# Optimization experiments

Hardware: AMD Instinct MI355X
Metric: run time of the kernel (lower is better)

## Reference

```python
import jax, jax.numpy as jnp
import numpy as np

B, T, F, H, O = 16384, 128, 9, 128, 12


def setup_inputs() -> dict:
    key = jax.random.key(0)
    ks = jax.random.split(key, 14)
    s = 1.0 / np.sqrt(H)
    u = lambda k, shp: jax.random.uniform(k, shp, jnp.float32, -s, s)
    return {
        "x": jax.random.normal(ks[0], (B, T, F), jnp.float32),
        "W_in": u(ks[1], (H, F)), "b_in": u(ks[2], (H,)),
        "Wih0": u(ks[3], (4 * H, H)), "Whh0": u(ks[4], (4 * H, H)),
        "bih0": u(ks[5], (4 * H,)), "bhh0": u(ks[6], (4 * H,)),
        "Wih1": u(ks[7], (4 * H, H)), "Whh1": u(ks[8], (4 * H, H)),
        "bih1": u(ks[9], (4 * H,)), "bhh1": u(ks[10], (4 * H,)),
        "W_out": u(ks[11], (O, H)), "b_out": u(ks[12], (O,)),
    }


def _cell(h, c, xp, Wih, Whh, bih, bhh):
    # PyTorch LSTM gate order: i, f, g, o
    g = xp @ Wih.T + bih + h @ Whh.T + bhh  # [B, 4H]
    i, f, gg, o = jnp.split(g, 4, axis=-1)
    c = jax.nn.sigmoid(f) * c + jax.nn.sigmoid(i) * jnp.tanh(gg)
    h = jax.nn.sigmoid(o) * jnp.tanh(c)
    return h, c


def reference(x, W_in, b_in, Wih0, Whh0, bih0, bhh0, Wih1, Whh1, bih1, bhh1, W_out, b_out):
    # input projection, all timesteps at once: [B, T, H] -> scan over time
    xp = jnp.einsum('btf,hf->tbh', x, W_in) + b_in
    b = x.shape[0]
    zeros = jnp.zeros((b, H), x.dtype)
    carry0 = (zeros, zeros, zeros, zeros)  # h0, c0, h1, c1

    def step(carry, xt):
        h0, c0, h1, c1 = carry
        h0, c0 = _cell(h0, c0, xt, Wih0, Whh0, bih0, bhh0)
        h1, c1 = _cell(h1, c1, h0, Wih1, Whh1, bih1, bhh1)
        return (h0, c0, h1, c1), None

    (h0, c0, h1, c1), _ = jax.lax.scan(step, carry0, xp)
    # torch forward returns only the LAST step's output: out(h1) with softmax over dim=1
    return jax.nn.softmax(h1 @ W_out.T + b_out, axis=1)
```

## Files before the change

kernel.cpp:

```cpp
#include <hip/hip_runtime.h>
#include <stdint.h>
#include <stddef.h>

#define T_STEPS 128
#define F_IN 9
#define HID 128
#define OUT_N 12
#define XROW (T_STEPS * F_IN)

typedef __attribute__((ext_vector_type(8))) short bf16x8;
typedef __attribute__((ext_vector_type(4))) float f32x4;

#define MFMA16(a, b, c) __builtin_amdgcn_mfma_f32_16x16x32_bf16((a), (b), (c), 0, 0, 0)

__device__ __forceinline__ short f2bf(float f) {
  union { float f; uint32_t u; } v; v.f = f;
  return (short)((v.u + 0x7fffu + ((v.u >> 16) & 1u)) >> 16);
}
__device__ __forceinline__ float frcp(float x) { return __builtin_amdgcn_rcpf(x); }
__device__ __forceinline__ float sigm(float x) {
  return frcp(1.0f + __builtin_amdgcn_exp2f(-1.4426950408889634f * x));
}
__device__ __forceinline__ float tanh_f(float x) {
  return 1.0f - 2.0f * frcp(1.0f + __builtin_amdgcn_exp2f(2.8853900817779268f * x));
}

__global__ void prep_w0x(const float* __restrict__ W_in, const float* __restrict__ b_in,
                         const float* __restrict__ Wih0, const float* __restrict__ bih0,
                         const float* __restrict__ bhh0, const float* __restrict__ bih1,
                         const float* __restrict__ bhh1,
                         short* __restrict__ w0xf, float* __restrict__ b0x, float* __restrict__ b1) {
  int tid = threadIdx.x;
  int nt = tid >> 4, hl = tid & 15;
  int w = nt >> 2, g = nt & 3;
  int n = g * 128 + w * 16 + hl;
  float wacc[F_IN];
#pragma unroll
  for (int f = 0; f < F_IN; ++f) wacc[f] = 0.f;
  float bacc = 0.f;
  for (int h = 0; h < HID; ++h) {
    float wv = Wih0[n * HID + h];
    bacc += wv * b_in[h];
#pragma unroll
    for (int f = 0; f < F_IN; ++f) wacc[f] += wv * W_in[h * F_IN + f];
  }
  b0x[n] = bacc + bih0[n] + bhh0[n];
  b1[n] = bih1[n] + bhh1[n];
#pragma unroll
  for (int k = 0; k < 32; ++k) {
    int quad = k >> 3, j = k & 7;
    w0xf[((w * 4 + g) * 64 + quad * 16 + hl) * 8 + j] = (k < F_IN) ? f2bf(wacc[k]) : (short)0;
  }
}

__global__ void prep_wrec(const float* __restrict__ Whh0, const float* __restrict__ Wih1,
                          const float* __restrict__ Whh1,
                          short* __restrict__ whh0f, short* __restrict__ w1f) {
  int gt = blockIdx.x * blockDim.x + threadIdx.x;
  if (gt < 2048) {
    int kt = gt >> 9, rr = gt & 511;
    int nt = rr >> 4, hl = rr & 15;
    int w = nt >> 2, g = nt & 3;
    int n = g * 128 + w * 16 + hl;
#pragma unroll
    for (int k = 0; k < 32; ++k) {
      int quad = k >> 3, j = k & 7;
      whh0f[((w * 16 + kt * 4 + g) * 64 + quad * 16 + hl) * 8 + j] =
          f2bf(Whh0[n * HID + kt * 32 + k]);
    }
  } else {
    int g2 = gt - 2048;
    int kt = g2 >> 9, rr = g2 & 511;
    int nt = rr >> 4, hl = rr & 15;
    int w = nt >> 2, g = nt & 3;
    int n = g * 128 + w * 16 + hl;
#pragma unroll
    for (int k = 0; k < 32; ++k) {
      int quad = k >> 3, j = k & 7;
      int kg = kt * 32 + k;
      float v = (kg < HID) ? Wih1[n * HID + kg] : Whh1[n * HID + kg - HID];
      w1f[((w * 32 + kt * 4 + g) * 64 + quad * 16 + hl) * 8 + j] = f2bf(v);
    }
  }
}

__global__ void __launch_bounds__(512) __attribute__((amdgpu_waves_per_eu(2)))
lstm_main(const float* __restrict__ x, const short* __restrict__ w0xf,
          const short* __restrict__ whh0f, const short* __restrict__ w1f,
          const float* __restrict__ b0x, const float* __restrict__ b1,
          const float* __restrict__ Wout, const float* __restrict__ bout,
          float* __restrict__ out) {
  __shared__ short sh[32768];
  __shared__ float h1fp[64 * HID];
  __shared__ float lg[64 * OUT_N];

  const int tid = threadIdx.x;
  const int w = tid >> 6, lane = tid & 63;
  const int quad = lane >> 4, c = lane & 15;
  const int rowbase = blockIdx.x * 64;

  {
    int* si = (int*)sh;
    for (int i = tid; i < 16384; i += 512) si[i] = 0;
  }

  short* h0_cur = sh;
  short* h0_prv = sh + 8192;
  short* h1_cur = sh + 16384;
  short* h1_prv = sh + 24576;

  float bias0[4], bias1[4];
#pragma unroll
  for (int g = 0; g < 4; ++g) {
    int n = g * 128 + w * 16 + c;
    bias0[g] = b0x[n];
    bias1[g] = b1[n];
  }

  const short* wp0 = w0xf + (w * 4) * 512 + lane * 8;
  const short* wph = whh0f + (w * 16) * 512 + lane * 8;
  const short* wp1 = w1f + (w * 32) * 512 + lane * 8;

  const int kt_w = w >> 1;
  const int klocal = ((w & 1) << 4) + c;
  const int quadA = klocal >> 3;
  const int jA = klocal & 7;
  const int wr_off = (kt_w * 64 + quadA * 16 + quad * 4) * 8 + jA;

  float c0[16], c1[16];
#pragma unroll
  for (int i = 0; i < 16; ++i) { c0[i] = 0.f; c1[i] = 0.f; }

  __syncthreads();

#pragma clang loop unroll(disable)
  for (int t = 0; t < T_STEPS; ++t) {
    bf16x8 xf[4];
#pragma unroll
    for (int mt = 0; mt < 4; ++mt) {
      bf16x8 v;
#pragma unroll
      for (int j = 0; j < 8; ++j) v[j] = 0;
      if (quad == 0) {
        const float* xp = x + (size_t)(rowbase + mt * 16 + c) * XROW + t * F_IN;
#pragma unroll
        for (int j = 0; j < 8; ++j) v[j] = f2bf(xp[j]);
      } else if (quad == 1) {
        v[0] = f2bf(x[(size_t)(rowbase + mt * 16 + c) * XROW + t * F_IN + 8]);
      }
      xf[mt] = v;
    }
    f32x4 acc[4][4];
#pragma unroll
    for (int mt = 0; mt < 4; ++mt)
#pragma unroll
      for (int g = 0; g < 4; ++g) {
        f32x4 a; a[0] = bias0[g]; a[1] = bias0[g]; a[2] = bias0[g]; a[3] = bias0[g];
        acc[mt][g] = a;
      }
    {
      bf16x8 b0_ = *(const bf16x8*)(wp0);
      bf16x8 b1_ = *(const bf16x8*)(wp0 + 512);
      bf16x8 b2_ = *(const bf16x8*)(wp0 + 1024);
      bf16x8 b3_ = *(const bf16x8*)(wp0 + 1536);
#pragma unroll
      for (int mt = 0; mt < 4; ++mt) {
        acc[mt][0] = MFMA16(xf[mt], b0_, acc[mt][0]);
        acc[mt][1] = MFMA16(xf[mt], b1_, acc[mt][1]);
        acc[mt][2] = MFMA16(xf[mt], b2_, acc[mt][2]);
        acc[mt][3] = MFMA16(xf[mt], b3_, acc[mt][3]);
      }
    }
#pragma clang loop unroll_count(2)
    for (int kt = 0; kt < 4; ++kt) {
      const short* wb = wph + kt * 2048;
      bf16x8 b0_ = *(const bf16x8*)(wb);
      bf16x8 b1_ = *(const bf16x8*)(wb + 512);
      bf16x8 b2_ = *(const bf16x8*)(wb + 1024);
      bf16x8 b3_ = *(const bf16x8*)(wb + 1536);
#pragma unroll
      for (int mt = 0; mt < 4; ++mt) {
        bf16x8 af = *(const bf16x8*)(h0_prv + ((mt * 4 + kt) * 64 + lane) * 8);
        acc[mt][0] = MFMA16(af, b0_, acc[mt][0]);
        acc[mt][1] = MFMA16(af, b1_, acc[mt][1]);
        acc[mt][2] = MFMA16(af, b2_, acc[mt][2]);
        acc[mt][3] = MFMA16(af, b3_, acc[mt][3]);
      }
    }
#pragma unroll
    for (int mt = 0; mt < 4; ++mt)
#pragma unroll
      for (int r = 0; r < 4; ++r) {
        float gi = sigm(acc[mt][0][r]);
        float gf = sigm(acc[mt][1][r]);
        float gg = tanh_f(acc[mt][2][r]);
        float go = sigm(acc[mt][3][r]);
        float cn = gf * c0[mt * 4 + r] + gi * gg;
        c0[mt * 4 + r] = cn;
        float hn = go * tanh_f(cn);
        h0_cur[mt * 2048 + r * 8 + wr_off] = f2bf(hn);
      }
    __syncthreads();
#pragma unroll
    for (int mt = 0; mt < 4; ++mt)
#pragma unroll
      for (int g = 0; g < 4; ++g) {
        f32x4 a; a[0] = bias1[g]; a[1] = bias1[g]; a[2] = bias1[g]; a[3] = bias1[g];
        acc[mt][g] = a;
      }
#pragma clang loop unroll_count(2)
    for (int kt = 0; kt < 4; ++kt) {
      const short* wb = wp1 + kt * 2048;
      bf16x8 b0_ = *(const bf16x8*)(wb);
      bf16x8 b1_ = *(const bf16x8*)(wb + 512);
      bf16x8 b2_ = *(const bf16x8*)(wb + 1024);
      bf16x8 b3_ = *(const bf16x8*)(wb + 1536);
#pragma unroll
      for (int mt = 0; mt < 4; ++mt) {
        bf16x8 af = *(const bf16x8*)(h0_cur + ((mt * 4 + kt) * 64 + lane) * 8);
        acc[mt][0] = MFMA16(af, b0_, acc[mt][0]);
        acc[mt][1] = MFMA16(af, b1_, acc[mt][1]);
        acc[mt][2] = MFMA16(af, b2_, acc[mt][2]);
        acc[mt][3] = MFMA16(af, b3_, acc[mt][3]);
      }
    }
#pragma clang loop unroll_count(2)
    for (int kt = 0; kt < 4; ++kt) {
      const short* wb = wp1 + (kt + 4) * 2048;
      bf16x8 b0_ = *(const bf16x8*)(wb);
      bf16x8 b1_ = *(const bf16x8*)(wb + 512);
      bf16x8 b2_ = *(const bf16x8*)(wb + 1024);
      bf16x8 b3_ = *(const bf16x8*)(wb + 1536);
#pragma unroll
      for (int mt = 0; mt < 4; ++mt) {
        bf16x8 af = *(const bf16x8*)(h1_prv + ((mt * 4 + kt) * 64 + lane) * 8);
        acc[mt][0] = MFMA16(af, b0_, acc[mt][0]);
        acc[mt][1] = MFMA16(af, b1_, acc[mt][1]);
        acc[mt][2] = MFMA16(af, b2_, acc[mt][2]);
        acc[mt][3] = MFMA16(af, b3_, acc[mt][3]);
      }
    }
#pragma unroll
    for (int mt = 0; mt < 4; ++mt)
#pragma unroll
      for (int r = 0; r < 4; ++r) {
        float gi = sigm(acc[mt][0][r]);
        float gf = sigm(acc[mt][1][r]);
        float gg = tanh_f(acc[mt][2][r]);
        float go = sigm(acc[mt][3][r]);
        float cn = gf * c1[mt * 4 + r] + gi * gg;
        c1[mt * 4 + r] = cn;
        float hn = go * tanh_f(cn);
        if (t == T_STEPS - 1) h1fp[(mt * 16 + quad * 4 + r) * HID + w * 16 + c] = hn;
        h1_cur[mt * 2048 + r * 8 + wr_off] = f2bf(hn);
      }
    __syncthreads();
    short* tp = h0_cur; h0_cur = h0_prv; h0_prv = tp;
    tp = h1_cur; h1_cur = h1_prv; h1_prv = tp;
  }

  {
    int row = tid >> 3, og = tid & 7;
    for (int oc = og; oc < OUT_N; oc += 8) {
      float s = bout[oc];
      const float* wo = Wout + oc * HID;
      const float* hr = h1fp + row * HID;
#pragma unroll 8
      for (int k = 0; k < HID; ++k) s += hr[k] * wo[k];
      lg[row * OUT_N + oc] = s;
    }
  }
  __syncthreads();
  if (tid < 64) {
    int row = tid;
    float m = lg[row * OUT_N];
#pragma unroll
    for (int oc = 1; oc < OUT_N; ++oc) m = fmaxf(m, lg[row * OUT_N + oc]);
    float e[OUT_N];
    float s = 0.f;
#pragma unroll
    for (int oc = 0; oc < OUT_N; ++oc) {
      e[oc] = __expf(lg[row * OUT_N + oc] - m);
      s += e[oc];
    }
    float inv = 1.0f / s;
    float* orow = out + (size_t)(rowbase + row) * OUT_N;
#pragma unroll
    for (int oc = 0; oc < OUT_N; ++oc) orow[oc] = e[oc] * inv;
  }
}

extern "C" void kernel_launch(void* const* d_in, const int* in_sizes, int n_in,
                              void* d_out, int out_size, void* d_ws, size_t ws_size,
                              hipStream_t stream) {
  const float* x    = (const float*)d_in[0];
  const float* W_in = (const float*)d_in[1];
  const float* b_in = (const float*)d_in[2];
  const float* Wih0 = (const float*)d_in[3];
  const float* Whh0 = (const float*)d_in[4];
  const float* bih0 = (const float*)d_in[5];
  const float* bhh0 = (const float*)d_in[6];
  const float* Wih1 = (const float*)d_in[7];
  const float* Whh1 = (const float*)d_in[8];
  const float* bih1 = (const float*)d_in[9];
  const float* bhh1 = (const float*)d_in[10];
  const float* Wout = (const float*)d_in[11];
  const float* bout = (const float*)d_in[12];
  float* out = (float*)d_out;

  short* w0xf  = (short*)d_ws;
  short* whh0f = w0xf + 16384;
  short* w1f   = whh0f + 65536;
  float* b0x   = (float*)(w1f + 131072);
  float* b1    = b0x + 512;

  prep_w0x<<<1, 512, 0, stream>>>(W_in, b_in, Wih0, bih0, bhh0, bih1, bhh1, w0xf, b0x, b1);
  prep_wrec<<<12, 512, 0, stream>>>(Whh0, Wih1, Whh1, whh0f, w1f);
  lstm_main<<<256, 512, 0, stream>>>(x, w0xf, whh0f, w1f, b0x, b1, Wout, bout, out);
}
```

Measured before the change: 1.397 ms.

## Halve rows per block to 32, double grid, target four waves per EU

Each block now handles 32 batch rows instead of 64, so the grid grows to 512 blocks and per-thread accumulators and cell state halve. The waves-per-EU hint rises to 4 so two blocks can share a CU and hide the per-step barrier and MFMA latency. Biases are folded into the exp2 argument via fma instead of seeding the accumulators, and wave-uniform weight pointers use readfirstlane. The cost is that every block streams the full weight set per timestep, so weight reads per row double, and register pressure under the tighter bound may cause spills.

```diff
diff --git a/kernel.cpp b/kernel.cpp
--- a/kernel.cpp
+++ b/kernel.cpp
@@ -18,11 +18,9 @@
   return (short)((v.u + 0x7fffu + ((v.u >> 16) & 1u)) >> 16);
 }
 __device__ __forceinline__ float frcp(float x) { return __builtin_amdgcn_rcpf(x); }
-__device__ __forceinline__ float sigm(float x) {
-  return frcp(1.0f + __builtin_amdgcn_exp2f(-1.4426950408889634f * x));
-}
+__device__ __forceinline__ float fexp2(float x) { return __builtin_amdgcn_exp2f(x); }
 __device__ __forceinline__ float tanh_f(float x) {
-  return 1.0f - 2.0f * frcp(1.0f + __builtin_amdgcn_exp2f(2.8853900817779268f * x));
+  return 1.0f - 2.0f * frcp(1.0f + fexp2(2.8853900817779268f * x));
 }
 
 __global__ void prep_w0x(const float* __restrict__ W_in, const float* __restrict__ b_in,
@@ -84,60 +82,66 @@
   }
 }
 
-__global__ void __launch_bounds__(512) __attribute__((amdgpu_waves_per_eu(2)))
+__global__ void __launch_bounds__(512) __attribute__((amdgpu_waves_per_eu(4, 4)))
 lstm_main(const float* __restrict__ x, const short* __restrict__ w0xf,
           const short* __restrict__ whh0f, const short* __restrict__ w1f,
           const float* __restrict__ b0x, const float* __restrict__ b1,
           const float* __restrict__ Wout, const float* __restrict__ bout,
           float* __restrict__ out) {
-  __shared__ short sh[32768];
-  __shared__ float h1fp[64 * HID];
-  __shared__ float lg[64 * OUT_N];
+  __shared__ short sh[16384];
+  __shared__ float h1fp[32 * HID];
+  __shared__ float lg[32 * OUT_N];
 
   const int tid = threadIdx.x;
   const int w = tid >> 6, lane = tid & 63;
   const int quad = lane >> 4, c = lane & 15;
-  const int rowbase = blockIdx.x * 64;
+  const int rowbase = blockIdx.x * 32;
 
   {
     int* si = (int*)sh;
-    for (int i = tid; i < 16384; i += 512) si[i] = 0;
+#pragma unroll
+    for (int i = 0; i < 16; ++i) si[tid + i * 512] = 0;
   }
 
   short* h0_cur = sh;
-  short* h0_prv = sh + 8192;
-  short* h1_cur = sh + 16384;
-  short* h1_prv = sh + 24576;
-
-  float bias0[4], bias1[4];
+  short* h0_prv = sh + 4096;
+  short* h1_cur = sh + 8192;
+  short* h1_prv = sh + 12288;
+
+  const int wu = __builtin_amdgcn_readfirstlane(w);
+  const short* wp0 = w0xf + wu * 4 * 512;
+  const short* wph = whh0f + wu * 16 * 512;
+  const short* wp1 = w1f + wu * 32 * 512;
+  const int lo = lane * 8;
+
+  float sb0[4], sb1[4];
 #pragma unroll
   for (int g = 0; g < 4; ++g) {
-    int n = g * 128 + w * 16 + c;
-    bias0[g] = b0x[n];
-    bias1[g] = b1[n];
-  }
-
-  const short* wp0 = w0xf + (w * 4) * 512 + lane * 8;
-  const short* wph = whh0f + (w * 16) * 512 + lane * 8;
-  const short* wp1 = w1f + (w * 32) * 512 + lane * 8;
-
-  const int kt_w = w >> 1;
-  const int klocal = ((w & 1) << 4) + c;
+    int n = g * 128 + wu * 16 + c;
+    float bv0 = b0x[n], bv1 = b1[n];
+    sb0[g] = (g == 2) ? 2.8853900817779268f * bv0 : -1.4426950408889634f * bv0;
+    sb1[g] = (g == 2) ? 2.8853900817779268f * bv1 : -1.4426950408889634f * bv1;
+  }
+
+  const int kt_w = wu >> 1;
+  const int klocal = ((wu & 1) << 4) + c;
   const int quadA = klocal >> 3;
   const int jA = klocal & 7;
   const int wr_off = (kt_w * 64 + quadA * 16 + quad * 4) * 8 + jA;
 
-  float c0[16], c1[16];
-#pragma unroll
-  for (int i = 0; i < 16; ++i) { c0[i] = 0.f; c1[i] = 0.f; }
+  float c0[8], c1[8];
+#pragma unroll
+  for (int i = 0; i < 8; ++i) { c0[i] = 0.f; c1[i] = 0.f; }
+
+  const f32x4 z4 = {0.f, 0.f, 0.f, 0.f};
 
   __syncthreads();
 
 #pragma clang loop unroll(disable)
   for (int t = 0; t < T_STEPS; ++t) {
-    bf16x8 xf[4];
-#pragma unroll
-    for (int mt = 0; mt < 4; ++mt) {
+    bf16x8 xf[2];
+#pragma unroll
+    for (int mt = 0; mt < 2; ++mt) {
       bf16x8 v;
 #pragma unroll
       for (int j = 0; j < 8; ++j) v[j] = 0;
@@ -150,36 +154,29 @@
       }
       xf[mt] = v;
     }
-    f32x4 acc[4][4];
-#pragma unroll
-    for (int mt = 0; mt < 4; ++mt)
-#pragma unroll
-      for (int g = 0; g < 4; ++g) {
-        f32x4 a; a[0] = bias0[g]; a[1] = bias0[g]; a[2] = bias0[g]; a[3] = bias0[g];
-        acc[mt][g] = a;
-      }
+    f32x4 acc[2][4];
     {
-      bf16x8 b0_ = *(const bf16x8*)(wp0);
-      bf16x8 b1_ = *(const bf16x8*)(wp0 + 512);
-      bf16x8 b2_ = *(const bf16x8*)(wp0 + 1024);
-      bf16x8 b3_ = *(const bf16x8*)(wp0 + 1536);
-#pragma unroll
-      for (int mt = 0; mt < 4; ++mt) {
-        acc[mt][0] = MFMA16(xf[mt], b0_, acc[mt][0]);
-        acc[mt][1] = MFMA16(xf[mt], b1_, acc[mt][1]);
-        acc[mt][2] = MFMA16(xf[mt], b2_, acc[mt][2]);
-        acc[mt][3] = MFMA16(xf[mt], b3_, acc[mt][3]);
-      }
-    }
-#pragma clang loop unroll_count(2)
+      bf16x8 b0_ = *(const bf16x8*)(wp0 + lo);
+      bf16x8 b1_ = *(const bf16x8*)(wp0 + lo + 512);
+      bf16x8 b2_ = *(const bf16x8*)(wp0 + lo + 1024);
+      bf16x8 b3_ = *(const bf16x8*)(wp0 + lo + 1536);
+#pragma unroll
+      for (int mt = 0; mt < 2; ++mt) {
+        acc[mt][0] = MFMA16(xf[mt], b0_, z4);
+        acc[mt][1] = MFMA16(xf[mt], b1_, z4);
+        acc[mt][2] = MFMA16(xf[mt], b2_, z4);
+        acc[mt][3] = MFMA16(xf[mt], b3_, z4);
+      }
+    }
+#pragma unroll
     for (int kt = 0; kt < 4; ++kt) {
-      const short* wb = wph + kt * 2048;
+      const short* wb = wph + lo + kt * 2048;
       bf16x8 b0_ = *(const bf16x8*)(wb);
       bf16x8 b1_ = *(const bf16x8*)(wb + 512);
       bf16x8 b2_ = *(const bf16x8*)(wb + 1024);
       bf16x8 b3_ = *(const bf16x8*)(wb + 1536);
 #pragma unroll
-      for (int mt = 0; mt < 4; ++mt) {
+      for (int mt = 0; mt < 2; ++mt) {
         bf16x8 af = *(const bf16x8*)(h0_prv + ((mt * 4 + kt) * 64 + lane) * 8);
         acc[mt][0] = MFMA16(af, b0_, acc[mt][0]);
         acc[mt][1] = MFMA16(af, b1_, acc[mt][1]);
@@ -188,35 +185,43 @@
       }
     }
 #pragma unroll
-    for (int mt = 0; mt < 4; ++mt)
+    for (int mt = 0; mt < 2; ++mt)
 #pragma unroll
       for (int r = 0; r < 4; ++r) {
-        float gi = sigm(acc[mt][0][r]);
-        float gf = sigm(acc[mt][1][r]);
-        float gg = tanh_f(acc[mt][2][r]);
-        float go = sigm(acc[mt][3][r]);
+        float gi = frcp(1.0f + fexp2(fmaf(-1.4426950408889634f, acc[mt][0][r], sb0[0])));
+        float gf = frcp(1.0f + fexp2(fmaf(-1.4426950408889634f, acc[mt][1][r], sb0[1])));
+        float gg = 1.0f - 2.0f * frcp(1.0f + fexp2(fmaf(2.8853900817779268f, acc[mt][2][r], sb0[2])));
+        float go = frcp(1.0f + fexp2(fmaf(-1.4426950408889634f, acc[mt][3][r], sb0[3])));
         float cn = gf * c0[mt * 4 + r] + gi * gg;
         c0[mt * 4 + r] = cn;
         float hn = go * tanh_f(cn);
         h0_cur[mt * 2048 + r * 8 + wr_off] = f2bf(hn);
       }
     __syncthreads();
-#pragma unroll
-    for (int mt = 0; mt < 4; ++mt)
-#pragma unroll
-      for (int g = 0; g < 4; ++g) {
-        f32x4 a; a[0] = bias1[g]; a[1] = bias1[g]; a[2] = bias1[g]; a[3] = bias1[g];
-        acc[mt][g] = a;
-      }
-#pragma clang loop unroll_count(2)
-    for (int kt = 0; kt < 4; ++kt) {
-      const short* wb = wp1 + kt * 2048;
+    {
+      const short* wb = wp1 + lo;
       bf16x8 b0_ = *(const bf16x8*)(wb);
       bf16x8 b1_ = *(const bf16x8*)(wb + 512);
       bf16x8 b2_ = *(const bf16x8*)(wb + 1024);
       bf16x8 b3_ = *(const bf16x8*)(wb + 1536);
 #pragma unroll
-      for (int mt = 0; mt < 4; ++mt) {
+      for (int mt = 0; mt < 2; ++mt) {
+        bf16x8 af = *(const bf16x8*)(h0_cur + ((mt * 4 + 0) * 64 + lane) * 8);
+        acc[mt][0] = MFMA16(af, b0_, z4);
+        acc[mt][1] = MFMA16(af, b1_, z4);
+        acc[mt][2] = MFMA16(af, b2_, z4);
+        acc[mt][3] = MFMA16(af, b3_, z4);
+      }
+    }
+#pragma unroll
+    for (int kt = 1; kt < 4; ++kt) {
+      const short* wb = wp1 + lo + kt * 2048;
+      bf16x8 b0_ = *(const bf16x8*)(wb);
+      bf16x8 b1_ = *(const bf16x8*)(wb + 512);
+      bf16x8 b2_ = *(const bf16x8*)(wb + 1024);
+      bf16x8 b3_ = *(const bf16x8*)(wb + 1536);
+#pragma unroll
+      for (int mt = 0; mt < 2; ++mt) {
         bf16x8 af = *(const bf16x8*)(h0_cur + ((mt * 4 + kt) * 64 + lane) * 8);
         acc[mt][0] = MFMA16(af, b0_, acc[mt][0]);
         acc[mt][1] = MFMA16(af, b1_, acc[mt][1]);
@@ -224,15 +229,15 @@
         acc[mt][3] = MFMA16(af, b3_, acc[mt][3]);
       }
     }
-#pragma clang loop unroll_count(2)
+#pragma unroll
     for (int kt = 0; kt < 4; ++kt) {
-      const short* wb = wp1 + (kt + 4) * 2048;
+      const short* wb = wp1 + lo + (kt + 4) * 2048;
       bf16x8 b0_ = *(const bf16x8*)(wb);
       bf16x8 b1_ = *(const bf16x8*)(wb + 512);
       bf16x8 b2_ = *(const bf16x8*)(wb + 1024);
       bf16x8 b3_ = *(const bf16x8*)(wb + 1536);
 #pragma unroll
-      for (int mt = 0; mt < 4; ++mt) {
+      for (int mt = 0; mt < 2; ++mt) {
         bf16x8 af = *(const bf16x8*)(h1_prv + ((mt * 4 + kt) * 64 + lane) * 8);
         acc[mt][0] = MFMA16(af, b0_, acc[mt][0]);
         acc[mt][1] = MFMA16(af, b1_, acc[mt][1]);
@@ -241,17 +246,17 @@
       }
     }
 #pragma unroll
-    for (int mt = 0; mt < 4; ++mt)
+    for (int mt = 0; mt < 2; ++mt)
 #pragma unroll
       for (int r = 0; r < 4; ++r) {
-        float gi = sigm(acc[mt][0][r]);
-        float gf = sigm(acc[mt][1][r]);
-        float gg = tanh_f(acc[mt][2][r]);
-        float go = sigm(acc[mt][3][r]);
+        float gi = frcp(1.0f + fexp2(fmaf(-1.4426950408889634f, acc[mt][0][r], sb1[0])));
+        float gf = frcp(1.0f + fexp2(fmaf(-1.4426950408889634f, acc[mt][1][r], sb1[1])));
+        float gg = 1.0f - 2.0f * frcp(1.0f + fexp2(fmaf(2.8853900817779268f, acc[mt][2][r], sb1[2])));
+        float go = frcp(1.0f + fexp2(fmaf(-1.4426950408889634f, acc[mt][3][r], sb1[3])));
         float cn = gf * c1[mt * 4 + r] + gi * gg;
         c1[mt * 4 + r] = cn;
         float hn = go * tanh_f(cn);
-        if (t == T_STEPS - 1) h1fp[(mt * 16 + quad * 4 + r) * HID + w * 16 + c] = hn;
+        if (t == T_STEPS - 1) h1fp[(mt * 16 + quad * 4 + r) * HID + wu * 16 + c] = hn;
         h1_cur[mt * 2048 + r * 8 + wr_off] = f2bf(hn);
       }
     __syncthreads();
@@ -260,18 +265,18 @@
   }
 
   {
-    int row = tid >> 3, og = tid & 7;
-    for (int oc = og; oc < OUT_N; oc += 8) {
-      float s = bout[oc];
-      const float* wo = Wout + oc * HID;
+    int row = tid >> 4, og = tid & 15;
+    if (og < OUT_N) {
+      float s = bout[og];
+      const float* wo = Wout + og * HID;
       const float* hr = h1fp + row * HID;
 #pragma unroll 8
       for (int k = 0; k < HID; ++k) s += hr[k] * wo[k];
-      lg[row * OUT_N + oc] = s;
+      lg[row * OUT_N + og] = s;
     }
   }
   __syncthreads();
-  if (tid < 64) {
+  if (tid < 32) {
     int row = tid;
     float m = lg[row * OUT_N];
 #pragma unroll
@@ -316,5 +321,5 @@
 
   prep_w0x<<<1, 512, 0, stream>>>(W_in, b_in, Wih0, bih0, bhh0, bih1, bhh1, w0xf, b0x, b1);
   prep_wrec<<<12, 512, 0, stream>>>(Whh0, Wih1, Whh1, whh0f, w1f);
-  lstm_main<<<256, 512, 0, stream>>>(x, w0xf, whh0f, w1f, b0x, b1, Wout, bout, out);
-}
+  lstm_main<<<512, 512, 0, stream>>>(x, w0xf, whh0f, w1f, b0x, b1, Wout, bout, out);
+}
```

After: 3.357 ms. 2.4x slower.

## Skew LSTM layers across timesteps to use one barrier per step

Applied to the files above, without the earlier changes.

Restructures the recurrence so layer 1 at step t-1 and layer 0 at step t are computed between the same pair of barriers, with a peeled prologue for layer 0 at t=0 and an epilogue for the final layer-1 step. This removes one of the two __syncthreads per timestep and the t==T-1 branch inside the loop. It also folds the log2(e) scaling into the bias (bias applied by fma before exp2, accumulators start at zero) and specializes the first step to skip the zero-state matmuls. The cost is more code and register pressure from the peeled stages, and the schedule is harder to keep correct.

```diff
diff --git a/kernel.cpp b/kernel.cpp
--- a/kernel.cpp
+++ b/kernel.cpp
@@ -18,11 +18,9 @@
   return (short)((v.u + 0x7fffu + ((v.u >> 16) & 1u)) >> 16);
 }
 __device__ __forceinline__ float frcp(float x) { return __builtin_amdgcn_rcpf(x); }
-__device__ __forceinline__ float sigm(float x) {
-  return frcp(1.0f + __builtin_amdgcn_exp2f(-1.4426950408889634f * x));
-}
+__device__ __forceinline__ float fexp2(float x) { return __builtin_amdgcn_exp2f(x); }
 __device__ __forceinline__ float tanh_f(float x) {
-  return 1.0f - 2.0f * frcp(1.0f + __builtin_amdgcn_exp2f(2.8853900817779268f * x));
+  return 1.0f - 2.0f * frcp(1.0f + fexp2(2.8853900817779268f * x));
 }
 
 __global__ void prep_w0x(const float* __restrict__ W_in, const float* __restrict__ b_in,
@@ -109,17 +107,18 @@
   short* h1_cur = sh + 16384;
   short* h1_prv = sh + 24576;
 
-  float bias0[4], bias1[4];
-#pragma unroll
-  for (int g = 0; g < 4; ++g) {
-    int n = g * 128 + w * 16 + c;
-    bias0[g] = b0x[n];
-    bias1[g] = b1[n];
-  }
-
   const short* wp0 = w0xf + (w * 4) * 512 + lane * 8;
   const short* wph = whh0f + (w * 16) * 512 + lane * 8;
   const short* wp1 = w1f + (w * 32) * 512 + lane * 8;
+
+  float sb0[4], sb1[4];
+#pragma unroll
+  for (int g = 0; g < 4; ++g) {
+    int n = g * 128 + w * 16 + c;
+    float bv0 = b0x[n], bv1 = b1[n];
+    sb0[g] = (g == 2) ? 2.8853900817779268f * bv0 : -1.4426950408889634f * bv0;
+    sb1[g] = (g == 2) ? 2.8853900817779268f * bv1 : -1.4426950408889634f * bv1;
+  }
 
   const int kt_w = w >> 1;
   const int klocal = ((w & 1) << 4) + c;
@@ -131,10 +130,11 @@
 #pragma unroll
   for (int i = 0; i < 16; ++i) { c0[i] = 0.f; c1[i] = 0.f; }
 
+  const f32x4 z4 = {0.f, 0.f, 0.f, 0.f};
+
   __syncthreads();
 
-#pragma clang loop unroll(disable)
-  for (int t = 0; t < T_STEPS; ++t) {
+  {
     bf16x8 xf[4];
 #pragma unroll
     for (int mt = 0; mt < 4; ++mt) {
@@ -142,22 +142,15 @@
 #pragma unroll
       for (int j = 0; j < 8; ++j) v[j] = 0;
       if (quad == 0) {
-        const float* xp = x + (size_t)(rowbase + mt * 16 + c) * XROW + t * F_IN;
+        const float* xp = x + (size_t)(rowbase + mt * 16 + c) * XROW;
 #pragma unroll
         for (int j = 0; j < 8; ++j) v[j] = f2bf(xp[j]);
       } else if (quad == 1) {
-        v[0] = f2bf(x[(size_t)(rowbase + mt * 16 + c) * XROW + t * F_IN + 8]);
+        v[0] = f2bf(x[(size_t)(rowbase + mt * 16 + c) * XROW + 8]);
       }
       xf[mt] = v;
     }
     f32x4 acc[4][4];
-#pragma unroll
-    for (int mt = 0; mt < 4; ++mt)
-#pragma unroll
-      for (int g = 0; g < 4; ++g) {
-        f32x4 a; a[0] = bias0[g]; a[1] = bias0[g]; a[2] = bias0[g]; a[3] = bias0[g];
-        acc[mt][g] = a;
-      }
     {
       bf16x8 b0_ = *(const bf16x8*)(wp0);
       bf16x8 b1_ = *(const bf16x8*)(wp0 + 512);
@@ -165,15 +158,182 @@
       bf16x8 b3_ = *(const bf16x8*)(wp0 + 1536);
 #pragma unroll
       for (int mt = 0; mt < 4; ++mt) {
-        acc[mt][0] = MFMA16(xf[mt], b0_, acc[mt][0]);
-        acc[mt][1] = MFMA16(xf[mt], b1_, acc[mt][1]);
-        acc[mt][2] = MFMA16(xf[mt], b2_, acc[mt][2]);
-        acc[mt][3] = MFMA16(xf[mt], b3_, acc[mt][3]);
-      }
-    }
+        acc[mt][0] = MFMA16(xf[mt], b0_, z4);
+        acc[mt][1] = MFMA16(xf[mt], b1_, z4);
+        acc[mt][2] = MFMA16(xf[mt], b2_, z4);
+        acc[mt][3] = MFMA16(xf[mt], b3_, z4);
+      }
+    }
+#pragma unroll
+    for (int mt = 0; mt < 4; ++mt)
+#pragma unroll
+      for (int r = 0; r < 4; ++r) {
+        float gi = frcp(1.0f + fexp2(fmaf(-1.4426950408889634f, acc[mt][0][r], sb0[0])));
+        float gf = frcp(1.0f + fexp2(fmaf(-1.4426950408889634f, acc[mt][1][r], sb0[1])));
+        float gg = 1.0f - 2.0f * frcp(1.0f + fexp2(fmaf(2.8853900817779268f, acc[mt][2][r], sb0[2])));
+        float go = frcp(1.0f + fexp2(fmaf(-1.4426950408889634f, acc[mt][3][r], sb0[3])));
+        float cn = gi * gg;
+        c0[mt * 4 + r] = cn;
+        float hn = go * tanh_f(cn);
+        h0_cur[mt * 2048 + r * 8 + wr_off] = f2bf(hn);
+      }
+  }
+  __syncthreads();
+  {
+    short* tp = h0_cur; h0_cur = h0_prv; h0_prv = tp;
+    tp = h1_cur; h1_cur = h1_prv; h1_prv = tp;
+  }
+
+#pragma clang loop unroll(disable)
+  for (int t = 1; t < T_STEPS; ++t) {
+    bf16x8 xf[4];
+#pragma unroll
+    for (int mt = 0; mt < 4; ++mt) {
+      bf16x8 v;
+#pragma unroll
+      for (int j = 0; j < 8; ++j) v[j] = 0;
+      if (quad == 0) {
+        const float* xp = x + (size_t)(rowbase + mt * 16 + c) * XROW + t * F_IN;
+#pragma unroll
+        for (int j = 0; j < 8; ++j) v[j] = f2bf(xp[j]);
+      } else if (quad == 1) {
+        v[0] = f2bf(x[(size_t)(rowbase + mt * 16 + c) * XROW + t * F_IN + 8]);
+      }
+      xf[mt] = v;
+    }
+    {
+      f32x4 acc[4][4];
+      {
+        const short* wb = wp1;
+        bf16x8 b0_ = *(const bf16x8*)(wb);
+        bf16x8 b1_ = *(const bf16x8*)(wb + 512);
+        bf16x8 b2_ = *(const bf16x8*)(wb + 1024);
+        bf16x8 b3_ = *(const bf16x8*)(wb + 1536);
+#pragma unroll
+        for (int mt = 0; mt < 4; ++mt) {
+          bf16x8 af = *(const bf16x8*)(h0_prv + ((mt * 4 + 0) * 64 + lane) * 8);
+          acc[mt][0] = MFMA16(af, b0_, z4);
+          acc[mt][1] = MFMA16(af, b1_, z4);
+          acc[mt][2] = MFMA16(af, b2_, z4);
+          acc[mt][3] = MFMA16(af, b3_, z4);
+        }
+      }
+#pragma clang loop unroll_count(3)
+      for (int kt = 1; kt < 4; ++kt) {
+        const short* wb = wp1 + kt * 2048;
+        bf16x8 b0_ = *(const bf16x8*)(wb);
+        bf16x8 b1_ = *(const bf16x8*)(wb + 512);
+        bf16x8 b2_ = *(const bf16x8*)(wb + 1024);
+        bf16x8 b3_ = *(const bf16x8*)(wb + 1536);
+#pragma unroll
+        for (int mt = 0; mt < 4; ++mt) {
+          bf16x8 af = *(const bf16x8*)(h0_prv + ((mt * 4 + kt) * 64 + lane) * 8);
+          acc[mt][0] = MFMA16(af, b0_, acc[mt][0]);
+          acc[mt][1] = MFMA16(af, b1_, acc[mt][1]);
+          acc[mt][2] = MFMA16(af, b2_, acc[mt][2]);
+          acc[mt][3] = MFMA16(af, b3_, acc[mt][3]);
+        }
+      }
 #pragma clang loop unroll_count(2)
-    for (int kt = 0; kt < 4; ++kt) {
-      const short* wb = wph + kt * 2048;
+      for (int kt = 0; kt < 4; ++kt) {
+        const short* wb = wp1 + (kt + 4) * 2048;
+        bf16x8 b0_ = *(const bf16x8*)(wb);
+        bf16x8 b1_ = *(const bf16x8*)(wb + 512);
+        bf16x8 b2_ = *(const bf16x8*)(wb + 1024);
+        bf16x8 b3_ = *(const bf16x8*)(wb + 1536);
+#pragma unroll
+        for (int mt = 0; mt < 4; ++mt) {
+          bf16x8 af = *(const bf16x8*)(h1_prv + ((mt * 4 + kt) * 64 + lane) * 8);
+          acc[mt][0] = MFMA16(af, b0_, acc[mt][0]);
+          acc[mt][1] = MFMA16(af, b1_, acc[mt][1]);
+          acc[mt][2] = MFMA16(af, b2_, acc[mt][2]);
+          acc[mt][3] = MFMA16(af, b3_, acc[mt][3]);
+        }
+      }
+#pragma unroll
+      for (int mt = 0; mt < 4; ++mt)
+#pragma unroll
+        for (int r = 0; r < 4; ++r) {
+          float gi = frcp(1.0f + fexp2(fmaf(-1.4426950408889634f, acc[mt][0][r], sb1[0])));
+          float gf = frcp(1.0f + fexp2(fmaf(-1.4426950408889634f, acc[mt][1][r], sb1[1])));
+          float gg = 1.0f - 2.0f * frcp(1.0f + fexp2(fmaf(2.8853900817779268f, acc[mt][2][r], sb1[2])));
+          float go = frcp(1.0f + fexp2(fmaf(-1.4426950408889634f, acc[mt][3][r], sb1[3])));
+          float cn = gf * c1[mt * 4 + r] + gi * gg;
+          c1[mt * 4 + r] = cn;
+          float hn = go * tanh_f(cn);
+          h1_cur[mt * 2048 + r * 8 + wr_off] = f2bf(hn);
+        }
+    }
+    {
+      f32x4 acc[4][4];
+      {
+        bf16x8 b0_ = *(const bf16x8*)(wp0);
+        bf16x8 b1_ = *(const bf16x8*)(wp0 + 512);
+        bf16x8 b2_ = *(const bf16x8*)(wp0 + 1024);
+        bf16x8 b3_ = *(const bf16x8*)(wp0 + 1536);
+#pragma unroll
+        for (int mt = 0; mt < 4; ++mt) {
+          acc[mt][0] = MFMA16(xf[mt], b0_, z4);
+          acc[mt][1] = MFMA16(xf[mt], b1_, z4);
+          acc[mt][2] = MFMA16(xf[mt], b2_, z4);
+          acc[mt][3] = MFMA16(xf[mt], b3_, z4);
+        }
+      }
+#pragma clang loop unroll_count(2)
+      for (int kt = 0; kt < 4; ++kt) {
+        const short* wb = wph + kt * 2048;
+        bf16x8 b0_ = *(const bf16x8*)(wb);
+        bf16x8 b1_ = *(const bf16x8*)(wb + 512);
+        bf16x8 b2_ = *(const bf16x8*)(wb + 1024);
+        bf16x8 b3_ = *(const bf16x8*)(wb + 1536);
+#pragma unroll
+        for (int mt = 0; mt < 4; ++mt) {
+          bf16x8 af = *(const bf16x8*)(h0_prv + ((mt * 4 + kt) * 64 + lane) * 8);
+          acc[mt][0] = MFMA16(af, b0_, acc[mt][0]);
+          acc[mt][1] = MFMA16(af, b1_, acc[mt][1]);
+          acc[mt][2] = MFMA16(af, b2_, acc[mt][2]);
+          acc[mt][3] = MFMA16(af, b3_, acc[mt][3]);
+        }
+      }
+#pragma unroll
+      for (int mt = 0; mt < 4; ++mt)
+#pragma unroll
+        for (int r = 0; r < 4; ++r) {
+          float gi = frcp(1.0f + fexp2(fmaf(-1.4426950408889634f, acc[mt][0][r], sb0[0])));
+          float gf = frcp(1.0f + fexp2(fmaf(-1.4426950408889634f, acc[mt][1][r], sb0[1])));
+          float gg = 1.0f - 2.0f * frcp(1.0f + fexp2(fmaf(2.8853900817779268f, acc[mt][2][r], sb0[2])));
+          float go = frcp(1.0f + fexp2(fmaf(-1.4426950408889634f, acc[mt][3][r], sb0[3])));
+          float cn = gf * c0[mt * 4 + r] + gi * gg;
+          c0[mt * 4 + r] = cn;
+          float hn = go * tanh_f(cn);
+          h0_cur[mt * 2048 + r * 8 + wr_off] = f2bf(hn);
+        }
+    }
+    __syncthreads();
+    short* tp = h0_cur; h0_cur = h0_prv; h0_prv = tp;
+    tp = h1_cur; h1_cur = h1_prv; h1_prv = tp;
+  }
+
+  {
+    f32x4 acc[4][4];
+    {
+      const short* wb = wp1;
+      bf16x8 b0_ = *(const bf16x8*)(wb);
+      bf16x8 b1_ = *(const bf16x8*)(wb + 512);
+      bf16x8 b2_ = *(const bf16x8*)(wb + 1024);
+      bf16x8 b3_ = *(const bf16x8*)(wb + 1536);
+#pragma unroll
+      for (int mt = 0; mt < 4; ++mt) {
+        bf16x8 af = *(const bf16x8*)(h0_prv + ((mt * 4 + 0) * 64 + lane) * 8);
+        acc[mt][0] = MFMA16(af, b0_, z4);
+        acc[mt][1] = MFMA16(af, b1_, z4);
+        acc[mt][2] = MFMA16(af, b2_, z4);
+        acc[mt][3] = MFMA16(af, b3_, z4);
+      }
+    }
+#pragma unroll
+    for (int kt = 1; kt < 4; ++kt) {
+      const short* wb = wp1 + kt * 2048;
       bf16x8 b0_ = *(const bf16x8*)(wb);
       bf16x8 b1_ = *(const bf16x8*)(wb + 512);
       bf16x8 b2_ = *(const bf16x8*)(wb + 1024);
@@ -188,43 +348,6 @@
       }
     }
 #pragma unroll
-    for (int mt = 0; mt < 4; ++mt)
-#pragma unroll
-      for (int r = 0; r < 4; ++r) {
-        float gi = sigm(acc[mt][0][r]);
-        float gf = sigm(acc[mt][1][r]);
-        float gg = tanh_f(acc[mt][2][r]);
-        float go = sigm(acc[mt][3][r]);
-        float cn = gf * c0[mt * 4 + r] + gi * gg;
-        c0[mt * 4 + r] = cn;
-        float hn = go * tanh_f(cn);
-        h0_cur[mt * 2048 + r * 8 + wr_off] = f2bf(hn);
-      }
-    __syncthreads();
-#pragma unroll
-    for (int mt = 0; mt < 4; ++mt)
-#pragma unroll
-      for (int g = 0; g < 4; ++g) {
-        f32x4 a; a[0] = bias1[g]; a[1] = bias1[g]; a[2] = bias1[g]; a[3] = bias1[g];
-        acc[mt][g] = a;
-      }
-#pragma clang loop unroll_count(2)
-    for (int kt = 0; kt < 4; ++kt) {
-      const short* wb = wp1 + kt * 2048;
-      bf16x8 b0_ = *(const bf16x8*)(wb);
-      bf16x8 b1_ = *(const bf16x8*)(wb + 512);
-      bf16x8 b2_ = *(const bf16x8*)(wb + 1024);
-      bf16x8 b3_ = *(const bf16x8*)(wb + 1536);
-#pragma unroll
-      for (int mt = 0; mt < 4; ++mt) {
-        bf16x8 af = *(const bf16x8*)(h0_cur + ((mt * 4 + kt) * 64 + lane) * 8);
-        acc[mt][0] = MFMA16(af, b0_, acc[mt][0]);
-        acc[mt][1] = MFMA16(af, b1_, acc[mt][1]);
-        acc[mt][2] = MFMA16(af, b2_, acc[mt][2]);
-        acc[mt][3] = MFMA16(af, b3_, acc[mt][3]);
-      }
-    }
-#pragma clang loop unroll_count(2)
     for (int kt = 0; kt < 4; ++kt) {
       const short* wb = wp1 + (kt + 4) * 2048;
       bf16x8 b0_ = *(const bf16x8*)(wb);
@@ -244,20 +367,16 @@
     for (int mt = 0; mt < 4; ++mt)
 #pragma unroll
       for (int r = 0; r < 4; ++r) {
-        float gi = sigm(acc[mt][0][r]);
-        float gf = sigm(acc[mt][1][r]);
-        float gg = tanh_f(acc[mt][2][r]);
-        float go = sigm(acc[mt][3][r]);
+        float gi = frcp(1.0f + fexp2(fmaf(-1.4426950408889634f, acc[mt][0][r], sb1[0])));
+        float gf = frcp(1.0f + fexp2(fmaf(-1.4426950408889634f, acc[mt][1][r], sb1[1])));
+        float gg = 1.0f - 2.0f * frcp(1.0f + fexp2(fmaf(2.8853900817779268f, acc[mt][2][r], sb1[2])));
+        float go = frcp(1.0f + fexp2(fmaf(-1.4426950408889634f, acc[mt][3][r], sb1[3])));
         float cn = gf * c1[mt * 4 + r] + gi * gg;
-        c1[mt * 4 + r] = cn;
         float hn = go * tanh_f(cn);
-        if (t == T_STEPS - 1) h1fp[(mt * 16 + quad * 4 + r) * HID + w * 16 + c] = hn;
-        h1_cur[mt * 2048 + r * 8 + wr_off] = f2bf(hn);
-      }
-    __syncthreads();
-    short* tp = h0_cur; h0_cur = h0_prv; h0_prv = tp;
-    tp = h1_cur; h1_cur = h1_prv; h1_prv = tp;
-  }
+        h1fp[(mt * 16 + quad * 4 + r) * HID + w * 16 + c] = hn;
+      }
+  }
+  __syncthreads();
 
   {
     int row = tid >> 3, og = tid & 7;
```

After: 1.341 ms. -4.0%, faster.
